# Kernel optimization log

Hardware: AMD Instinct MI355X
Metric: run time of the kernel (lower is better)

The kernel has to match this reference:

```python
import jax, jax.numpy as jnp
import numpy as np

N_NODES = 100000
N_EDGES = 1600000
IN_DIM = 128
HID = 128
N_CLASSES = 16
N_GRAPHS = 512


def setup_inputs() -> dict:
    key = jax.random.key(0)
    ks = jax.random.split(key, 16)
    d = {
        "x": jax.random.normal(ks[0], (N_NODES, IN_DIM), jnp.float32),
        "src": jax.random.randint(ks[1], (N_EDGES,), 0, N_NODES, jnp.int64 if jax.config.jax_enable_x64 else jnp.int32),
        "dst": jax.random.randint(ks[2], (N_EDGES,), 0, N_NODES, jnp.int64 if jax.config.jax_enable_x64 else jnp.int32),
        "gid": jnp.sort(jax.random.randint(ks[3], (N_NODES,), 0, N_GRAPHS, jnp.int64 if jax.config.jax_enable_x64 else jnp.int32)),
    }
    s = 1.0 / np.sqrt(HID)
    for i, k in zip(range(1, 5), ks[4:8]):
        d[f"W{i}"] = jax.random.uniform(k, (HID, HID), jnp.float32, -s, s)
        d[f"b{i}"] = jnp.zeros((HID,), jnp.float32)
    d["Wv"] = jax.random.uniform(ks[8], (HID, 1), jnp.float32, -s, s)
    d["bv"] = jnp.zeros((1,), jnp.float32)
    d["Wc"] = jax.random.uniform(ks[9], (HID, N_CLASSES), jnp.float32, -s, s)
    d["bc"] = jnp.zeros((N_CLASSES,), jnp.float32)
    return d


def _gcn_layer(h, W, b, src, dst, norm_src, norm_dst):
    # DGL GraphConv, norm='both': D_dst^{-1/2} * A * D_src^{-1/2} * h * W + b, then ReLU outside
    m = (h * norm_src[:, None])[src]                                  # [E, H] edge gather
    agg = jax.ops.segment_sum(m, dst, num_segments=N_NODES)           # [N, H] scatter-add
    return jax.nn.relu(agg * norm_dst[:, None] @ W + b)


def reference(x, W1, b1, W2, b2, W3, b3, W4, b4, Wv, bv, Wc, bc, src, dst, gid):
    ones = jnp.ones((N_EDGES,), jnp.float32)
    deg_out = jnp.clip(jax.ops.segment_sum(ones, src, num_segments=N_NODES), 1.0)
    deg_in = jnp.clip(jax.ops.segment_sum(ones, dst, num_segments=N_NODES), 1.0)
    norm_src = jax.lax.rsqrt(deg_out)
    norm_dst = jax.lax.rsqrt(deg_in)

    h = _gcn_layer(x, W1, b1, src, dst, norm_src, norm_dst)
    h = _gcn_layer(h, W2, b2, src, dst, norm_src, norm_dst)
    h = _gcn_layer(h, W3, b3, src, dst, norm_src, norm_dst)
    h = _gcn_layer(h, W4, b4, src, dst, norm_src, norm_dst)

    w = jax.nn.sigmoid(h @ Wv + bv)                                   # [N, 1]
    num = jax.ops.segment_sum(h * w, gid, num_segments=N_GRAPHS)      # [G, H]
    den = jax.ops.segment_sum(w, gid, num_segments=N_GRAPHS)          # [G, 1]
    hg = jnp.where(den > 0, num / jnp.where(den > 0, den, 1.0), 0.0)  # weighted mean readout
    return hg @ Wc + bc                                               # [G, n_classes]
```

## Files before the change

kernel.cpp:

```cpp
#include <hip/hip_runtime.h>
#include <hip/hip_bf16.h>

#define N_NODES_C 100000
#define N_EDGES_C 1600000
#define HID_C 128
#define NCLS_C 16
#define NGRAPH_C 512
#define ELL_CAP 64
#define PREP_GROUPS 8
#define PREP_RANGE ((N_NODES_C + PREP_GROUPS - 1) / PREP_GROUPS)
#define PREP_GB 256
#define PREP_CHUNK (N_EDGES_C / PREP_GB)

#define GEMM_BLOCKS ((N_NODES_C + 127) / 128)
#define PREP_BLOCKS (PREP_GROUPS * PREP_GB)
#define GS_BLOCKS ((N_NODES_C + 255) / 256)
#define FRONT_BLOCKS (GEMM_BLOCKS + PREP_BLOCKS + GS_BLOCKS)

__device__ __forceinline__ void gemm_body(
    const float* __restrict__ A, const float* __restrict__ W,
    float* __restrict__ U, int m0, float (*sA)[132], float (*sB)[132]) {
  int t = threadIdx.x;
  int tx = t & 15, ty = t >> 4;

  float acc[8][8];
#pragma unroll
  for (int i = 0; i < 8; ++i)
#pragma unroll
    for (int j = 0; j < 8; ++j) acc[i][j] = 0.f;

  int a_c4 = (t & 7) * 4;
  int a_r = t >> 3;
  int w_n4 = (t & 31) * 4;
  int w_k = t >> 5;

  for (int k0 = 0; k0 < HID_C; k0 += 32) {
#pragma unroll
    for (int rr = 0; rr < 4; ++rr) {
      int r = rr * 32 + a_r;
      int row = m0 + r;
      float4 v = make_float4(0.f, 0.f, 0.f, 0.f);
      if (row < N_NODES_C) v = *(const float4*)&A[(size_t)row * HID_C + k0 + a_c4];
      sA[a_c4 + 0][r] = v.x;
      sA[a_c4 + 1][r] = v.y;
      sA[a_c4 + 2][r] = v.z;
      sA[a_c4 + 3][r] = v.w;
    }
#pragma unroll
    for (int i = 0; i < 4; ++i) {
      int kc = i * 8 + w_k;
      float4 v = *(const float4*)&W[(size_t)(k0 + kc) * HID_C + w_n4];
      *(float4*)&sB[kc][w_n4] = v;
    }
    __syncthreads();

#pragma unroll 4
    for (int kk = 0; kk < 32; ++kk) {
      float4 a0 = *(const float4*)&sA[kk][ty * 8];
      float4 a1 = *(const float4*)&sA[kk][ty * 8 + 4];
      float4 bb0 = *(const float4*)&sB[kk][tx * 8];
      float4 bb1 = *(const float4*)&sB[kk][tx * 8 + 4];
      float a[8] = {a0.x, a0.y, a0.z, a0.w, a1.x, a1.y, a1.z, a1.w};
      float b[8] = {bb0.x, bb0.y, bb0.z, bb0.w, bb1.x, bb1.y, bb1.z, bb1.w};
#pragma unroll
      for (int i = 0; i < 8; ++i)
#pragma unroll
        for (int j = 0; j < 8; ++j) acc[i][j] = fmaf(a[i], b[j], acc[i][j]);
    }
    __syncthreads();
  }

#pragma unroll
  for (int i = 0; i < 8; ++i) {
    int row = m0 + ty * 8 + i;
    if (row < N_NODES_C) {
      float4 v0 = {acc[i][0], acc[i][1], acc[i][2], acc[i][3]};
      float4 v1 = {acc[i][4], acc[i][5], acc[i][6], acc[i][7]};
      float4* p = (float4*)&U[(size_t)row * HID_C + tx * 8];
      p[0] = v0;
      p[1] = v1;
    }
  }
}

__global__ __launch_bounds__(256) void k_front(
    const float* __restrict__ x, const float* __restrict__ W1,
    float* __restrict__ U1, const int* __restrict__ src,
    const int* __restrict__ dst, int* cnt_out, int* cursor,
    int* __restrict__ ell, const int* __restrict__ gid,
    int* __restrict__ gstart) {
  __shared__ float sA[32][132];
  __shared__ float sB[32][132];
  int bid = blockIdx.x;
  if (bid < GEMM_BLOCKS) {
    gemm_body(x, W1, U1, bid * 128, sA, sB);
  } else if (bid < GEMM_BLOCKS + PREP_BLOCKS) {
    int grp = bid & (PREP_GROUPS - 1);
    int gb = (bid - GEMM_BLOCKS) >> 3;
    int lo = grp * PREP_RANGE;
    int e0 = gb * PREP_CHUNK;
    int e1 = e0 + PREP_CHUNK;
    for (int i = e0 + threadIdx.x; i < e1; i += 256) {
      int s = src[i];
      int d = dst[i];
      if ((unsigned)(s - lo) < (unsigned)PREP_RANGE) atomicAdd(&cnt_out[s], 1);
      if ((unsigned)(d - lo) < (unsigned)PREP_RANGE) {
        int p = atomicAdd(&cursor[d], 1);
        if (p < ELL_CAP) ell[((size_t)d << 6) + p] = s;
      }
    }
  } else {
    int n = (bid - GEMM_BLOCKS - PREP_BLOCKS) * 256 + threadIdx.x;
    if (n >= N_NODES_C) return;
    int g = gid[n];
    int gp = (n == 0) ? -1 : gid[n - 1];
    for (int k = gp + 1; k <= g; ++k) gstart[k] = n;
    if (n == N_NODES_C - 1) {
      for (int k = g + 1; k <= NGRAPH_C; ++k) gstart[k] = N_NODES_C;
    }
  }
}

__global__ __launch_bounds__(256) void k_gemm(
    const float* __restrict__ A, const float* __restrict__ W,
    float* __restrict__ U) {
  __shared__ float sA[32][132];
  __shared__ float sB[32][132];
  gemm_body(A, W, U, blockIdx.x * 128, sA, sB);
}

__global__ __launch_bounds__(256) void k_agg(
    const float* __restrict__ U, const int* __restrict__ cnt_in,
    const int* __restrict__ cnt_out, const int* __restrict__ ell,
    const float* __restrict__ bias, float* __restrict__ H) {
  int wid = threadIdx.x >> 6, lane = threadIdx.x & 63;
  int half = lane >> 5, li = lane & 31;
  int n = blockIdx.x * 4 + wid;
  if (n >= N_NODES_C) return;
  const int* lst = ell + ((size_t)n << 6);
  int degfull = cnt_in[n];
  int deg = degfull > ELL_CAP ? ELL_CAP : degfull;
  const float4* U4 = (const float4*)U;
  float4 acc = make_float4(0.f, 0.f, 0.f, 0.f);
  int e = 0;
  for (; e + 8 <= deg; e += 8) {
    int i0 = lst[e + 0 + half], i1 = lst[e + 2 + half];
    int i2 = lst[e + 4 + half], i3 = lst[e + 6 + half];
    float s0 = 1.f / sqrtf((float)cnt_out[i0]);
    float s1 = 1.f / sqrtf((float)cnt_out[i1]);
    float s2 = 1.f / sqrtf((float)cnt_out[i2]);
    float s3 = 1.f / sqrtf((float)cnt_out[i3]);
    float4 v0 = U4[(size_t)i0 * 32 + li];
    float4 v1 = U4[(size_t)i1 * 32 + li];
    float4 v2 = U4[(size_t)i2 * 32 + li];
    float4 v3 = U4[(size_t)i3 * 32 + li];
    acc.x = fmaf(v0.x, s0, fmaf(v1.x, s1, fmaf(v2.x, s2, fmaf(v3.x, s3, acc.x))));
    acc.y = fmaf(v0.y, s0, fmaf(v1.y, s1, fmaf(v2.y, s2, fmaf(v3.y, s3, acc.y))));
    acc.z = fmaf(v0.z, s0, fmaf(v1.z, s1, fmaf(v2.z, s2, fmaf(v3.z, s3, acc.z))));
    acc.w = fmaf(v0.w, s0, fmaf(v1.w, s1, fmaf(v2.w, s2, fmaf(v3.w, s3, acc.w))));
  }
  for (; e + 2 <= deg; e += 2) {
    int i = lst[e + half];
    float s = 1.f / sqrtf((float)cnt_out[i]);
    float4 v = U4[(size_t)i * 32 + li];
    acc.x = fmaf(v.x, s, acc.x);
    acc.y = fmaf(v.y, s, acc.y);
    acc.z = fmaf(v.z, s, acc.z);
    acc.w = fmaf(v.w, s, acc.w);
  }
  if (e < deg) {
    int i = lst[e];
    float s = 1.f / sqrtf((float)cnt_out[i]);
    float4 v = U4[(size_t)i * 32 + li];
    if (half == 0) {
      acc.x = fmaf(v.x, s, acc.x);
      acc.y = fmaf(v.y, s, acc.y);
      acc.z = fmaf(v.z, s, acc.z);
      acc.w = fmaf(v.w, s, acc.w);
    }
  }
  acc.x += __shfl_xor(acc.x, 32);
  acc.y += __shfl_xor(acc.y, 32);
  acc.z += __shfl_xor(acc.z, 32);
  acc.w += __shfl_xor(acc.w, 32);
  if (half == 0) {
    float nd = 1.f / sqrtf(fmaxf((float)degfull, 1.f));
    float4 bb = ((const float4*)bias)[li];
    float4 r;
    r.x = fmaxf(fmaf(acc.x, nd, bb.x), 0.f);
    r.y = fmaxf(fmaf(acc.y, nd, bb.y), 0.f);
    r.z = fmaxf(fmaf(acc.z, nd, bb.z), 0.f);
    r.w = fmaxf(fmaf(acc.w, nd, bb.w), 0.f);
    ((float4*)H)[(size_t)n * 32 + li] = r;
  }
}

__global__ __launch_bounds__(256) void k_readout(
    const float* __restrict__ H, const float* __restrict__ Wv,
    const float* __restrict__ bv, const int* __restrict__ gstart,
    const float* __restrict__ Wc, const float* __restrict__ bc,
    float* __restrict__ out) {
  int g = blockIdx.x;
  int wid = threadIdx.x >> 6, lane = threadIdx.x & 63;
  int s0 = gstart[g], s1 = gstart[g + 1];
  float2 wv2 = ((const float2*)Wv)[lane];
  float bvs = bv[0];
  float ax = 0.f, ay = 0.f, dw = 0.f;
  for (int n = s0 + wid; n < s1; n += 4) {
    float2 h2 = ((const float2*)H)[(size_t)n * 64 + lane];
    float p = h2.x * wv2.x + h2.y * wv2.y;
#pragma unroll
    for (int off = 32; off > 0; off >>= 1) p += __shfl_xor(p, off);
    float w = 1.f / (1.f + expf(-(p + bvs)));
    ax += h2.x * w;
    ay += h2.y * w;
    dw += w;
  }
  __shared__ float2 snum[4][64];
  __shared__ float sden[4];
  __shared__ float hg[HID_C];
  snum[wid][lane] = make_float2(ax, ay);
  if (lane == 0) sden[wid] = dw;
  __syncthreads();
  if (wid == 0) {
    float2 a = snum[0][lane], b = snum[1][lane], c = snum[2][lane], d = snum[3][lane];
    float den = sden[0] + sden[1] + sden[2] + sden[3];
    float inv = (den > 0.f) ? 1.f / den : 0.f;
    hg[2 * lane] = (a.x + b.x + c.x + d.x) * inv;
    hg[2 * lane + 1] = (a.y + b.y + c.y + d.y) * inv;
  }
  __syncthreads();
  if (threadIdx.x < NCLS_C) {
    int c = threadIdx.x;
    float acc = 0.f;
    for (int k = 0; k < HID_C; ++k) acc = fmaf(hg[k], Wc[k * NCLS_C + c], acc);
    out[g * NCLS_C + c] = acc + bc[c];
  }
}

extern "C" void kernel_launch(void* const* d_in, const int* in_sizes, int n_in,
                              void* d_out, int out_size, void* d_ws, size_t ws_size,
                              hipStream_t stream) {
  const float* x = (const float*)d_in[0];
  const int* src = (const int*)d_in[1];
  const int* dst = (const int*)d_in[2];
  const int* gid = (const int*)d_in[3];
  const float* W[4] = {(const float*)d_in[4], (const float*)d_in[6],
                       (const float*)d_in[8], (const float*)d_in[10]};
  const float* b[4] = {(const float*)d_in[5], (const float*)d_in[7],
                       (const float*)d_in[9], (const float*)d_in[11]};
  const float* Wv = (const float*)d_in[12];
  const float* bv = (const float*)d_in[13];
  const float* Wc = (const float*)d_in[14];
  const float* bc = (const float*)d_in[15];
  float* out = (float*)d_out;

  char* ws = (char*)d_ws;
  size_t off = 0;
  auto alloc = [&](size_t bytes) -> char* {
    char* p = ws + off;
    off = (off + bytes + 255) & ~(size_t)255;
    return p;
  };
  int* cnt_out = (int*)alloc((size_t)N_NODES_C * 4);
  int* cursor = (int*)alloc((size_t)N_NODES_C * 4);
  int* gstart = (int*)alloc((size_t)(NGRAPH_C + 1) * 4);
  int* ell = (int*)alloc((size_t)N_NODES_C * ELL_CAP * 4);
  float* bufU = (float*)alloc((size_t)N_NODES_C * HID_C * 4);
  float* bufH = (float*)alloc((size_t)N_NODES_C * HID_C * 4);
  (void)ws_size;
  (void)in_sizes;
  (void)n_in;
  (void)out_size;

  hipMemsetAsync(cnt_out, 0, (size_t)N_NODES_C * 4, stream);
  hipMemsetAsync(cursor, 0, (size_t)N_NODES_C * 4, stream);

  k_front<<<FRONT_BLOCKS, 256, 0, stream>>>(x, W[0], bufU, src, dst, cnt_out,
                                            cursor, ell, gid, gstart);

  int node_grid = (N_NODES_C + 3) / 4;
  k_agg<<<node_grid, 256, 0, stream>>>(bufU, cursor, cnt_out, ell, b[0], bufH);
  for (int l = 1; l < 4; ++l) {
    k_gemm<<<GEMM_BLOCKS, 256, 0, stream>>>(bufH, W[l], bufU);
    k_agg<<<node_grid, 256, 0, stream>>>(bufU, cursor, cnt_out, ell, b[l], bufH);
  }

  k_readout<<<NGRAPH_C, 256, 0, stream>>>(bufH, Wv, bv, gstart, Wc, bc, out);
}
```

Baseline: 811.0 us.

## Build ELL adjacency via two-pass bucketing with shared-memory atomics

Replaces the edge-preprocessing step, which re-scanned all edges once per node-range group and did global atomics on per-node counters. Now each edge is read once and appended into coarse node-range buckets, replicated eight ways to spread atomic contention. A new kernel then places each bucket's edges into the ELL rows and computes degree counts using shared-memory atomics. This removes repeated edge reads and scattered global per-node atomics, at the cost of an extra kernel launch, extra bucket buffers, and a fixed per-bucket capacity that could overflow on skewed graphs.

```diff
diff --git a/kernel.cpp b/kernel.cpp
--- a/kernel.cpp
+++ b/kernel.cpp
@@ -7,15 +7,16 @@
 #define NCLS_C 16
 #define NGRAPH_C 512
 #define ELL_CAP 64
-#define PREP_GROUPS 8
-#define PREP_RANGE ((N_NODES_C + PREP_GROUPS - 1) / PREP_GROUPS)
-#define PREP_GB 256
-#define PREP_CHUNK (N_EDGES_C / PREP_GB)
+
+#define NBKT 256
+#define NRANGE 391
+#define RCAP 1024
+#define NREP 8
 
 #define GEMM_BLOCKS ((N_NODES_C + 127) / 128)
-#define PREP_BLOCKS (PREP_GROUPS * PREP_GB)
+#define B1_BLOCKS 1024
 #define GS_BLOCKS ((N_NODES_C + 255) / 256)
-#define FRONT_BLOCKS (GEMM_BLOCKS + PREP_BLOCKS + GS_BLOCKS)
+#define FRONT_BLOCKS (B1_BLOCKS + GEMM_BLOCKS + GS_BLOCKS)
 
 __device__ __forceinline__ void gemm_body(
     const float* __restrict__ A, const float* __restrict__ W,
@@ -86,31 +87,30 @@
 __global__ __launch_bounds__(256) void k_front(
     const float* __restrict__ x, const float* __restrict__ W1,
     float* __restrict__ U1, const int* __restrict__ src,
-    const int* __restrict__ dst, int* cnt_out, int* cursor,
-    int* __restrict__ ell, const int* __restrict__ gid,
+    const int* __restrict__ dst, int* bcur, int2* __restrict__ dstbkt,
+    int* __restrict__ srcbkt, const int* __restrict__ gid,
     int* __restrict__ gstart) {
   __shared__ float sA[32][132];
   __shared__ float sB[32][132];
   int bid = blockIdx.x;
-  if (bid < GEMM_BLOCKS) {
-    gemm_body(x, W1, U1, bid * 128, sA, sB);
-  } else if (bid < GEMM_BLOCKS + PREP_BLOCKS) {
-    int grp = bid & (PREP_GROUPS - 1);
-    int gb = (bid - GEMM_BLOCKS) >> 3;
-    int lo = grp * PREP_RANGE;
-    int e0 = gb * PREP_CHUNK;
-    int e1 = e0 + PREP_CHUNK;
-    for (int i = e0 + threadIdx.x; i < e1; i += 256) {
+  if (bid < B1_BLOCKS) {
+    int r = bid & (NREP - 1);
+    int i = bid * 256 + threadIdx.x;
+    int stride = B1_BLOCKS * 256;
+    for (; i < N_EDGES_C; i += stride) {
       int s = src[i];
       int d = dst[i];
-      if ((unsigned)(s - lo) < (unsigned)PREP_RANGE) atomicAdd(&cnt_out[s], 1);
-      if ((unsigned)(d - lo) < (unsigned)PREP_RANGE) {
-        int p = atomicAdd(&cursor[d], 1);
-        if (p < ELL_CAP) ell[((size_t)d << 6) + p] = s;
-      }
-    }
+      int bd = d / NRANGE;
+      int pd = atomicAdd(&bcur[bd * NREP + r], 1);
+      if (pd < RCAP) dstbkt[((bd * NREP + r) << 10) + pd] = make_int2(d, s);
+      int bs = s / NRANGE;
+      int ps = atomicAdd(&bcur[NBKT * NREP + bs * NREP + r], 1);
+      if (ps < RCAP) srcbkt[((bs * NREP + r) << 10) + ps] = s;
+    }
+  } else if (bid < B1_BLOCKS + GEMM_BLOCKS) {
+    gemm_body(x, W1, U1, (bid - B1_BLOCKS) * 128, sA, sB);
   } else {
-    int n = (bid - GEMM_BLOCKS - PREP_BLOCKS) * 256 + threadIdx.x;
+    int n = (bid - B1_BLOCKS - GEMM_BLOCKS) * 256 + threadIdx.x;
     if (n >= N_NODES_C) return;
     int g = gid[n];
     int gp = (n == 0) ? -1 : gid[n - 1];
@@ -118,6 +118,52 @@
     if (n == N_NODES_C - 1) {
       for (int k = g + 1; k <= NGRAPH_C; ++k) gstart[k] = N_NODES_C;
     }
+  }
+}
+
+__global__ __launch_bounds__(256) void k_build(
+    const int* __restrict__ bcur, const int2* __restrict__ dstbkt,
+    const int* __restrict__ srcbkt, int* __restrict__ ell,
+    int* __restrict__ cnt_in, int* __restrict__ cnt_out) {
+  __shared__ int lcur[NRANGE];
+  int tid = threadIdx.x;
+  int bid = blockIdx.x;
+  for (int t = tid; t < NRANGE; t += 256) lcur[t] = 0;
+  __syncthreads();
+  if (bid < NBKT) {
+    int b = bid;
+    int lo = b * NRANGE;
+    int nr = N_NODES_C - lo;
+    if (nr > NRANGE) nr = NRANGE;
+#pragma unroll 1
+    for (int r = 0; r < NREP; ++r) {
+      int len = bcur[b * NREP + r];
+      if (len > RCAP) len = RCAP;
+      const int2* slice = dstbkt + ((size_t)(b * NREP + r) << 10);
+      for (int j = tid; j < len; j += 256) {
+        int2 e = slice[j];
+        int p = atomicAdd(&lcur[e.x - lo], 1);
+        if (p < ELL_CAP) ell[((size_t)e.x << 6) + p] = e.y;
+      }
+    }
+    __syncthreads();
+    for (int t = tid; t < nr; t += 256) cnt_in[lo + t] = lcur[t];
+  } else {
+    int b = bid - NBKT;
+    int lo = b * NRANGE;
+    int nr = N_NODES_C - lo;
+    if (nr > NRANGE) nr = NRANGE;
+#pragma unroll 1
+    for (int r = 0; r < NREP; ++r) {
+      int len = bcur[NBKT * NREP + b * NREP + r];
+      if (len > RCAP) len = RCAP;
+      const int* slice = srcbkt + ((size_t)(b * NREP + r) << 10);
+      for (int j = tid; j < len; j += 256) {
+        atomicAdd(&lcur[slice[j] - lo], 1);
+      }
+    }
+    __syncthreads();
+    for (int t = tid; t < nr; t += 256) cnt_out[lo + t] = lcur[t];
   }
 }
 
@@ -263,9 +309,12 @@
     return p;
   };
   int* cnt_out = (int*)alloc((size_t)N_NODES_C * 4);
-  int* cursor = (int*)alloc((size_t)N_NODES_C * 4);
+  int* cnt_in = (int*)alloc((size_t)N_NODES_C * 4);
   int* gstart = (int*)alloc((size_t)(NGRAPH_C + 1) * 4);
+  int* bcur = (int*)alloc((size_t)2 * NBKT * NREP * 4);
   int* ell = (int*)alloc((size_t)N_NODES_C * ELL_CAP * 4);
+  int2* dstbkt = (int2*)alloc((size_t)NBKT * NREP * RCAP * 8);
+  int* srcbkt = (int*)alloc((size_t)NBKT * NREP * RCAP * 4);
   float* bufU = (float*)alloc((size_t)N_NODES_C * HID_C * 4);
   float* bufH = (float*)alloc((size_t)N_NODES_C * HID_C * 4);
   (void)ws_size;
@@ -273,17 +322,17 @@
   (void)n_in;
   (void)out_size;
 
-  hipMemsetAsync(cnt_out, 0, (size_t)N_NODES_C * 4, stream);
-  hipMemsetAsync(cursor, 0, (size_t)N_NODES_C * 4, stream);
-
-  k_front<<<FRONT_BLOCKS, 256, 0, stream>>>(x, W[0], bufU, src, dst, cnt_out,
-                                            cursor, ell, gid, gstart);
+  hipMemsetAsync(bcur, 0, (size_t)2 * NBKT * NREP * 4, stream);
+
+  k_front<<<FRONT_BLOCKS, 256, 0, stream>>>(x, W[0], bufU, src, dst, bcur,
+                                            dstbkt, srcbkt, gid, gstart);
+  k_build<<<2 * NBKT, 256, 0, stream>>>(bcur, dstbkt, srcbkt, ell, cnt_in, cnt_out);
 
   int node_grid = (N_NODES_C + 3) / 4;
-  k_agg<<<node_grid, 256, 0, stream>>>(bufU, cursor, cnt_out, ell, b[0], bufH);
+  k_agg<<<node_grid, 256, 0, stream>>>(bufU, cnt_in, cnt_out, ell, b[0], bufH);
   for (int l = 1; l < 4; ++l) {
     k_gemm<<<GEMM_BLOCKS, 256, 0, stream>>>(bufH, W[l], bufU);
-    k_agg<<<node_grid, 256, 0, stream>>>(bufU, cursor, cnt_out, ell, b[l], bufH);
+    k_agg<<<node_grid, 256, 0, stream>>>(bufU, cnt_in, cnt_out, ell, b[l], bufH);
   }
 
   k_readout<<<NGRAPH_C, 256, 0, stream>>>(bufH, Wv, bv, gstart, Wc, bc, out);
```

New measurement: 973.8 us. +20.1%, slower.

## Bind edge-prep node ranges to the executing XCD via hardware ID and work queue

Applied to the files above, without the earlier changes.

The preprocessing blocks now read the hardware XCC ID and handle only the destination/source node range owned by that XCD. Each block pulls edge chunks from a per-XCD atomic work counter, so every XCD covers all edges for its range whatever the block-to-XCD mapping is. The aim is to keep each atomic counter and ELL row in one XCD's L2 and cut cross-die atomic traffic. In exchange it adds a shared-memory handoff with two block barriers per chunk and one more memset.

```diff
diff --git a/kernel.cpp b/kernel.cpp
--- a/kernel.cpp
+++ b/kernel.cpp
@@ -7,13 +7,13 @@
 #define NCLS_C 16
 #define NGRAPH_C 512
 #define ELL_CAP 64
-#define PREP_GROUPS 8
-#define PREP_RANGE ((N_NODES_C + PREP_GROUPS - 1) / PREP_GROUPS)
+#define NXCD 8
+#define XCD_RANGE ((N_NODES_C + NXCD - 1) / NXCD)
 #define PREP_GB 256
 #define PREP_CHUNK (N_EDGES_C / PREP_GB)
 
 #define GEMM_BLOCKS ((N_NODES_C + 127) / 128)
-#define PREP_BLOCKS (PREP_GROUPS * PREP_GB)
+#define PREP_BLOCKS 2048
 #define GS_BLOCKS ((N_NODES_C + 255) / 256)
 #define FRONT_BLOCKS (GEMM_BLOCKS + PREP_BLOCKS + GS_BLOCKS)
 
@@ -87,26 +87,35 @@
     const float* __restrict__ x, const float* __restrict__ W1,
     float* __restrict__ U1, const int* __restrict__ src,
     const int* __restrict__ dst, int* cnt_out, int* cursor,
-    int* __restrict__ ell, const int* __restrict__ gid,
+    int* __restrict__ ell, int* xcd_cnt, const int* __restrict__ gid,
     int* __restrict__ gstart) {
   __shared__ float sA[32][132];
   __shared__ float sB[32][132];
+  __shared__ int s_chunk;
   int bid = blockIdx.x;
   if (bid < GEMM_BLOCKS) {
     gemm_body(x, W1, U1, bid * 128, sA, sB);
   } else if (bid < GEMM_BLOCKS + PREP_BLOCKS) {
-    int grp = bid & (PREP_GROUPS - 1);
-    int gb = (bid - GEMM_BLOCKS) >> 3;
-    int lo = grp * PREP_RANGE;
-    int e0 = gb * PREP_CHUNK;
-    int e1 = e0 + PREP_CHUNK;
-    for (int i = e0 + threadIdx.x; i < e1; i += 256) {
-      int s = src[i];
-      int d = dst[i];
-      if ((unsigned)(s - lo) < (unsigned)PREP_RANGE) atomicAdd(&cnt_out[s], 1);
-      if ((unsigned)(d - lo) < (unsigned)PREP_RANGE) {
-        int p = atomicAdd(&cursor[d], 1);
-        if (p < ELL_CAP) ell[((size_t)d << 6) + p] = s;
+    unsigned int xcd;
+    asm volatile("s_getreg_b32 %0, hwreg(HW_REG_XCC_ID)" : "=s"(xcd));
+    xcd &= (NXCD - 1);
+    int lo = (int)xcd * XCD_RANGE;
+    for (;;) {
+      if (threadIdx.x == 0) s_chunk = atomicAdd(&xcd_cnt[xcd], 1);
+      __syncthreads();
+      int chunk = s_chunk;
+      __syncthreads();
+      if (chunk >= PREP_GB) break;
+      int e0 = chunk * PREP_CHUNK;
+      int e1 = e0 + PREP_CHUNK;
+      for (int i = e0 + threadIdx.x; i < e1; i += 256) {
+        int s = src[i];
+        int d = dst[i];
+        if ((unsigned)(s - lo) < (unsigned)XCD_RANGE) atomicAdd(&cnt_out[s], 1);
+        if ((unsigned)(d - lo) < (unsigned)XCD_RANGE) {
+          int p = atomicAdd(&cursor[d], 1);
+          if (p < ELL_CAP) ell[((size_t)d << 6) + p] = s;
+        }
       }
     }
   } else {
@@ -265,6 +274,7 @@
   int* cnt_out = (int*)alloc((size_t)N_NODES_C * 4);
   int* cursor = (int*)alloc((size_t)N_NODES_C * 4);
   int* gstart = (int*)alloc((size_t)(NGRAPH_C + 1) * 4);
+  int* xcd_cnt = (int*)alloc((size_t)NXCD * 4);
   int* ell = (int*)alloc((size_t)N_NODES_C * ELL_CAP * 4);
   float* bufU = (float*)alloc((size_t)N_NODES_C * HID_C * 4);
   float* bufH = (float*)alloc((size_t)N_NODES_C * HID_C * 4);
@@ -275,9 +285,10 @@
 
   hipMemsetAsync(cnt_out, 0, (size_t)N_NODES_C * 4, stream);
   hipMemsetAsync(cursor, 0, (size_t)N_NODES_C * 4, stream);
+  hipMemsetAsync(xcd_cnt, 0, (size_t)NXCD * 4, stream);
 
   k_front<<<FRONT_BLOCKS, 256, 0, stream>>>(x, W[0], bufU, src, dst, cnt_out,
-                                            cursor, ell, gid, gstart);
+                                            cursor, ell, xcd_cnt, gid, gstart);
 
   int node_grid = (N_NODES_C + 3) / 4;
   k_agg<<<node_grid, 256, 0, stream>>>(bufU, cursor, cnt_out, ell, b[0], bufH);
```

Result: no change. 817.9 us (+0.9%).
